# Performance work log

Hardware: AMD Instinct MI355X
Metric: run time of the kernel (lower is better)

The kernel has to match this reference:

```python
import jax, jax.numpy as jnp
import numpy as np

SHAPE = (160, 160, 160)  # spatial grid (D, H, W)
N_VOX = 400_000
C_IN, C_OUT, K = 32, 64, 3


def setup_inputs() -> dict:
    key = jax.random.key(0)
    k1, k2, k3 = jax.random.split(key, 3)
    # unique active voxel coords (batch=0, z, y, x)
    rng = np.random.default_rng(0)
    flat = rng.choice(SHAPE[0] * SHAPE[1] * SHAPE[2], size=N_VOX, replace=False)
    z, y, x = np.unravel_index(flat, SHAPE)
    coors = np.stack([np.zeros(N_VOX, np.int32), z.astype(np.int32), y.astype(np.int32), x.astype(np.int32)], axis=1)
    features = jax.random.normal(k1, (N_VOX, C_IN), dtype=jnp.float32)
    weight = jax.random.normal(k2, (K * K * K, C_IN, C_OUT), dtype=jnp.float32) * (1.0 / np.sqrt(C_IN * K * K * K))
    bias = jax.random.normal(k3, (C_OUT,), dtype=jnp.float32) * 0.01
    return {"features": features, "coors": jnp.asarray(coors), "weight": weight, "bias": bias, "batch_size": 1}


def reference(features, coors, weight, bias, batch_size):
    # Submanifold sparse 3D conv: output coords == input coords.
    n = features.shape[0]
    b, z, y, x = coors[:, 0], coors[:, 1], coors[:, 2], coors[:, 3]
    D, H, W = SHAPE
    # dense voxel->row index lookup grid (the "hash map" for rulebook build)
    grid = jnp.full((batch_size, D, H, W), -1, dtype=jnp.int32)
    grid = grid.at[b, z, y, x].set(jnp.arange(n, dtype=jnp.int32))
    out = jnp.broadcast_to(bias, (n, C_OUT)).astype(features.dtype)
    k = 0
    for dz in (-1, 0, 1):
        for dy in (-1, 0, 1):
            for dx in (-1, 0, 1):
                nz, ny, nx = z + dz, y + dy, x + dx
                inb = (nz >= 0) & (nz < D) & (ny >= 0) & (ny < H) & (nx >= 0) & (nx < W)
                idx = grid[b, jnp.clip(nz, 0, D - 1), jnp.clip(ny, 0, H - 1), jnp.clip(nx, 0, W - 1)]
                valid = inb & (idx >= 0)
                gathered = jnp.where(valid[:, None], features[jnp.clip(idx, 0)], 0.0)  # [n, C_IN]
                out = out + gathered @ weight[k]  # small GEMM per kernel offset
                k += 1
    return out
```

## Files before the change

### kernel.cpp

```cpp
#include <hip/hip_runtime.h>
#include <stdint.h>

#define DD 160
#define HH 160
#define WW 160
#define NGRID (DD*HH*WW)
#define NCHUNK (NGRID/1024)
#define CIN 32
#define COUT 64
#define KK 27
#define BLOCK 1024
#define WPB 16
#define NBLOCKS 256
#define TOTW (NBLOCKS*WPB)
#define M27 0x07FFFFFFu

typedef _Float16 h2_t __attribute__((ext_vector_type(2)));

__device__ __forceinline__ h2_t as_h2(uint32_t u) {
    union { uint32_t u; h2_t h; } c; c.u = u; return c.h;
}
__device__ __forceinline__ uint32_t f2h(float f) {
    union { _Float16 h; uint16_t u; } c; c.h = (_Float16)f; return (uint32_t)c.u;
}

__device__ __forceinline__ float dot2(uint32_t fu, uint32_t wu, float acc) {
#if defined(__has_builtin)
#if __has_builtin(__builtin_amdgcn_fdot2)
    return __builtin_amdgcn_fdot2(as_h2(fu), as_h2(wu), acc, false);
#else
    h2_t f = as_h2(fu), w = as_h2(wu);
    acc = fmaf((float)f.x, (float)w.x, acc);
    return fmaf((float)f.y, (float)w.y, acc);
#endif
#else
    h2_t f = as_h2(fu), w = as_h2(wu);
    acc = fmaf((float)f.x, (float)w.x, acc);
    return fmaf((float)f.y, (float)w.y, acc);
#endif
}

__global__ void scatter_pack(const int4* __restrict__ coors, const float* __restrict__ w,
                             int* __restrict__ grid, int* __restrict__ cnt,
                             uint4* __restrict__ wpk, int n)
{
    int gid = blockIdx.x * 256 + threadIdx.x;
    if (gid < n) {
        int4 c = coors[gid];
        int cell = (c.y*HH + c.z)*WW + c.w;
        grid[cell] = gid;
        atomicAdd(&cnt[cell >> 10], 1);
    } else if (gid < n + KK*4*COUT) {
        int t = gid - n;
        int co = t & 63;
        int g  = (t >> 6) & 3;
        int k  = t >> 8;
        const float* base = w + (size_t)k*CIN*COUT + (size_t)(8*g)*COUT + co;
        uint4 r;
        r.x = f2h(base[0*COUT]) | (f2h(base[1*COUT]) << 16);
        r.y = f2h(base[2*COUT]) | (f2h(base[3*COUT]) << 16);
        r.z = f2h(base[4*COUT]) | (f2h(base[5*COUT]) << 16);
        r.w = f2h(base[6*COUT]) | (f2h(base[7*COUT]) << 16);
        wpk[t] = r;
    }
}

__global__ __launch_bounds__(1024) void scan_chunks(const int* __restrict__ cnt,
                                                    int* __restrict__ base)
{
    __shared__ int s[1024];
    int t = threadIdx.x;
    int c0 = 0, c1 = 0, c2 = 0, c3 = 0, sum;
    int i0 = t * 4;
    if (i0 + 3 < NCHUNK) { c0 = cnt[i0]; c1 = cnt[i0+1]; c2 = cnt[i0+2]; c3 = cnt[i0+3]; }
    else {
        if (i0     < NCHUNK) c0 = cnt[i0];
        if (i0 + 1 < NCHUNK) c1 = cnt[i0+1];
        if (i0 + 2 < NCHUNK) c2 = cnt[i0+2];
        if (i0 + 3 < NCHUNK) c3 = cnt[i0+3];
    }
    sum = c0 + c1 + c2 + c3;
    s[t] = sum; __syncthreads();
    for (int off = 1; off < 1024; off <<= 1) {
        int val = (t >= off) ? s[t - off] : 0;
        __syncthreads();
        s[t] += val;
        __syncthreads();
    }
    int excl = s[t] - sum;
    if (i0     < NCHUNK) { base[i0]   = excl; excl += c0; }
    if (i0 + 1 < NCHUNK) { base[i0+1] = excl; excl += c1; }
    if (i0 + 2 < NCHUNK) { base[i0+2] = excl; excl += c2; }
    if (i0 + 3 < NCHUNK) { base[i0+3] = excl; }
}

__global__ __launch_bounds__(1024) void emit_sort(const float4* __restrict__ f4,
                                                  int* __restrict__ grid,
                                                  const int* __restrict__ base,
                                                  int* __restrict__ pos, int* __restrict__ om,
                                                  uint2* __restrict__ fh)
{
    __shared__ int wt[16];
    int cell = blockIdx.x * 1024 + threadIdx.x;
    int g = grid[cell];
    bool pres = g >= 0;
    unsigned long long bal = __ballot(pres);
    int lane = threadIdx.x & 63;
    int wv = threadIdx.x >> 6;
    int lpre = __popcll(bal & ((1ull << lane) - 1ull));
    if (lane == 0) wt[wv] = __popcll(bal);
    __syncthreads();
    if (threadIdx.x == 0) {
        int acc = 0;
        for (int i = 0; i < 16; ++i) { int c = wt[i]; wt[i] = acc; acc += c; }
    }
    __syncthreads();
    if (pres) {
        int sp = base[blockIdx.x] + wt[wv] + lpre;
        pos[sp] = cell;
        om[sp]  = g;
        grid[cell] = sp;
        const float4* src = f4 + (size_t)g * 8;
        uint2* dst = fh + (size_t)sp * 8;
        #pragma unroll
        for (int q = 0; q < 8; ++q) {
            float4 vv = src[q];
            uint2 r;
            r.x = f2h(vv.x) | (f2h(vv.y) << 16);
            r.y = f2h(vv.z) | (f2h(vv.w) << 16);
            dst[q] = r;
        }
    }
}

#define LOAD4(D0,D1,D2,D3,J) { \
    const uint4* fp_ = fh4 + (size_t)(J) * 4; \
    D0 = fp_[0]; D1 = fp_[1]; D2 = fp_[2]; D3 = fp_[3]; }

#define MAC4(F0,F1,F2,F3,kk) { \
    const uint4* wl_ = wlds + (size_t)(kk)*4*COUT + lane; \
    uint4 w0_ = wl_[0], w1_ = wl_[COUT], w2_ = wl_[2*COUT], w3_ = wl_[3*COUT]; \
    a0 = dot2(F0.x, w0_.x, a0); a1 = dot2(F0.y, w0_.y, a1); \
    a2 = dot2(F0.z, w0_.z, a2); a3 = dot2(F0.w, w0_.w, a3); \
    a0 = dot2(F1.x, w1_.x, a0); a1 = dot2(F1.y, w1_.y, a1); \
    a2 = dot2(F1.z, w1_.z, a2); a3 = dot2(F1.w, w1_.w, a3); \
    a0 = dot2(F2.x, w2_.x, a0); a1 = dot2(F2.y, w2_.y, a1); \
    a2 = dot2(F2.z, w2_.z, a2); a3 = dot2(F2.w, w2_.w, a3); \
    a0 = dot2(F3.x, w3_.x, a0); a1 = dot2(F3.y, w3_.y, a1); \
    a2 = dot2(F3.z, w3_.z, a2); a3 = dot2(F3.w, w3_.w, a3); }

__global__ __launch_bounds__(BLOCK, 4) void sparse_conv(
    const uint4* __restrict__ fh4, const int* __restrict__ pos, const int* __restrict__ om,
    const float* __restrict__ bias, const uint4* __restrict__ wpk,
    const int* __restrict__ grid, float* __restrict__ out, int n, int run)
{
    extern __shared__ uint4 wlds[];

    for (int t = threadIdx.x; t < KK*4*COUT; t += BLOCK)
        wlds[t] = wpk[t];
    __syncthreads();

    const int lane = threadIdx.x & 63;
    const int wave = __builtin_amdgcn_readfirstlane((int)(threadIdx.x >> 6));
    const int b0 = blockIdx.x;
    const int sw = ((b0 & 7) << 5) + (b0 >> 3);
    const int wg = sw * WPB + wave;
    const int lo = wg * run;
    const int hi = min(n, lo + run);

    const float b = bias[lane];
    const int pl = lane & 31;
    const bool prober = pl < KK;
    const int dz = pl / 9 - 1;
    const int dy = (pl / 3) % 3 - 1;
    const int dx = pl % 3 - 1;
    const int hioff = (lane >= 32) ? 1 : 0;

    int nidx = -1;

    auto probe = [&](int pb) -> int {
        int r = -1;
        int pv = pb + hioff;
        if (prober && pv < hi) {
            int cell = pos[pv];
            int z = cell / (HH*WW); int rem = cell % (HH*WW);
            int y = rem / WW;       int x = rem % WW;
            int nz = z + dz, ny = y + dy, nx = x + dx;
            if (nz >= 0 && nz < DD && ny >= 0 && ny < HH && nx >= 0 && nx < WW)
                r = grid[(nz*HH + ny)*WW + nx];
        }
        return r;
    };

    auto runvox = [&](uint32_t m, int base, int orig) {
        float a0 = 0.f, a1 = 0.f, a2 = 0.f, a3 = 0.f;
        uint4 A0, A1, A2, A3, B0, B1, B2, B3;
        int kA = __ffs(m) - 1; m &= m - 1;
        int jA = __builtin_amdgcn_readlane(nidx, base + kA);
        LOAD4(A0, A1, A2, A3, jA);
        for (;;) {
            if (!m) { MAC4(A0, A1, A2, A3, kA); break; }
            int kB = __ffs(m) - 1; m &= m - 1;
            int jB = __builtin_amdgcn_readlane(nidx, base + kB);
            LOAD4(B0, B1, B2, B3, jB);
            MAC4(A0, A1, A2, A3, kA);
            if (!m) { MAC4(B0, B1, B2, B3, kB); break; }
            kA = __ffs(m) - 1; m &= m - 1;
            jA = __builtin_amdgcn_readlane(nidx, base + kA);
            LOAD4(A0, A1, A2, A3, jA);
            MAC4(B0, B1, B2, B3, kB);
        }
        float r = b + ((a0 + a1) + (a2 + a3));
        __builtin_nontemporal_store(r, out + (size_t)orig * COUT + lane);
    };

    int v = lo;
    nidx = probe(v);

    while (v < hi) {
        unsigned long long bal = __ballot(nidx >= 0);
        int nidx_next = probe(v + 2);

        uint32_t mA = (uint32_t)bal & M27;
        uint32_t mB = (uint32_t)(bal >> 32) & M27;

        runvox(mA, 0, om[v]);
        if (v + 1 < hi) runvox(mB, 32, om[v + 1]);

        v += 2;
        nidx = nidx_next;
    }
}

extern "C" void kernel_launch(void* const* d_in, const int* in_sizes, int n_in,
                              void* d_out, int out_size, void* d_ws, size_t ws_size,
                              hipStream_t stream) {
    const float* feats  = (const float*)d_in[0];
    const int*   coors  = (const int*)d_in[1];
    const float* weight = (const float*)d_in[2];
    const float* bias   = (const float*)d_in[3];
    float*       outp   = (float*)d_out;

    const int n = in_sizes[1] / 4;

    char* ws = (char*)d_ws;
    int*   grid = (int*)ws;                                   ws += (size_t)NGRID * 4;
    int*   cnt  = (int*)ws;                                   ws += (size_t)NCHUNK * 4;
    int*   base = (int*)ws;                                   ws += (size_t)NCHUNK * 4;
    uint4* wpk  = (uint4*)ws;                                 ws += (size_t)KK * 4 * COUT * 16;
    int*   pos  = (int*)ws;                                   ws += (size_t)n * 4;
    int*   om   = (int*)ws;                                   ws += (size_t)n * 4;
    uint2* fh   = (uint2*)ws;

    hipMemsetAsync(grid, 0xFF, (size_t)NGRID * 4, stream);
    hipMemsetAsync(cnt, 0, (size_t)NCHUNK * 4, stream);

    scatter_pack<<<(n + KK*4*COUT + 255) / 256, 256, 0, stream>>>(
        (const int4*)coors, weight, grid, cnt, wpk, n);

    scan_chunks<<<1, 1024, 0, stream>>>(cnt, base);

    emit_sort<<<NCHUNK, 1024, 0, stream>>>((const float4*)feats, grid, base, pos, om, fh);

    const int run = (n + TOTW - 1) / TOTW;
    const size_t lds = (size_t)KK * 4 * COUT * sizeof(uint4);
    sparse_conv<<<NBLOCKS, BLOCK, lds, stream>>>((const uint4*)fh, pos, om,
                                                 bias, wpk, grid, outp, n, run);
}
```

Before: 365.3 us.

## Replace per-voxel fdot2 accumulation with 16-voxel MFMA tiles over all taps

The conv kernel now processes groups of 16 sorted voxels per wave and computes all 27 taps densely with 16x16x32 f16 MFMA instructions, instead of walking each voxel's neighbor bitmask with fdot2. Missing neighbors point to a zero feature row appended after the features, which scatter_pack now writes, so the loop needs no branches. Weights are repacked in MFMA B-operand layout, and neighbor probes for the next group are prefetched and distributed with ds_bpermute. The aim is to trade wasted dense work on roughly 90% empty taps for much higher matrix throughput and regular control flow. Voxel counts not divisible by 16 would leave a tail unprocessed.

```diff
diff --git a/kernel.cpp b/kernel.cpp
--- a/kernel.cpp
+++ b/kernel.cpp
@@ -13,36 +13,19 @@
 #define WPB 16
 #define NBLOCKS 256
 #define TOTW (NBLOCKS*WPB)
-#define M27 0x07FFFFFFu
-
-typedef _Float16 h2_t __attribute__((ext_vector_type(2)));
-
-__device__ __forceinline__ h2_t as_h2(uint32_t u) {
-    union { uint32_t u; h2_t h; } c; c.u = u; return c.h;
-}
+
+typedef _Float16 f16x8 __attribute__((ext_vector_type(8)));
+typedef float f32x4 __attribute__((ext_vector_type(4)));
+
+union FU { uint4 u; f16x8 h; };
+
 __device__ __forceinline__ uint32_t f2h(float f) {
     union { _Float16 h; uint16_t u; } c; c.h = (_Float16)f; return (uint32_t)c.u;
 }
 
-__device__ __forceinline__ float dot2(uint32_t fu, uint32_t wu, float acc) {
-#if defined(__has_builtin)
-#if __has_builtin(__builtin_amdgcn_fdot2)
-    return __builtin_amdgcn_fdot2(as_h2(fu), as_h2(wu), acc, false);
-#else
-    h2_t f = as_h2(fu), w = as_h2(wu);
-    acc = fmaf((float)f.x, (float)w.x, acc);
-    return fmaf((float)f.y, (float)w.y, acc);
-#endif
-#else
-    h2_t f = as_h2(fu), w = as_h2(wu);
-    acc = fmaf((float)f.x, (float)w.x, acc);
-    return fmaf((float)f.y, (float)w.y, acc);
-#endif
-}
-
 __global__ void scatter_pack(const int4* __restrict__ coors, const float* __restrict__ w,
                              int* __restrict__ grid, int* __restrict__ cnt,
-                             uint4* __restrict__ wpk, int n)
+                             uint4* __restrict__ wpk, uint2* __restrict__ fh, int n)
 {
     int gid = blockIdx.x * 256 + threadIdx.x;
     if (gid < n) {
@@ -50,18 +33,21 @@
         int cell = (c.y*HH + c.z)*WW + c.w;
         grid[cell] = gid;
         atomicAdd(&cnt[cell >> 10], 1);
-    } else if (gid < n + KK*4*COUT) {
+    } else if (gid < n + KK*4*64) {
         int t = gid - n;
-        int co = t & 63;
-        int g  = (t >> 6) & 3;
-        int k  = t >> 8;
-        const float* base = w + (size_t)k*CIN*COUT + (size_t)(8*g)*COUT + co;
+        int l = t & 63, tile = (t >> 6) & 3, k = t >> 8;
+        int col = tile*16 + (l & 15);
+        int k0 = (l >> 4) * 8;
+        const float* base = w + (size_t)k*CIN*COUT + col;
         uint4 r;
-        r.x = f2h(base[0*COUT]) | (f2h(base[1*COUT]) << 16);
-        r.y = f2h(base[2*COUT]) | (f2h(base[3*COUT]) << 16);
-        r.z = f2h(base[4*COUT]) | (f2h(base[5*COUT]) << 16);
-        r.w = f2h(base[6*COUT]) | (f2h(base[7*COUT]) << 16);
+        r.x = f2h(base[(k0+0)*COUT]) | (f2h(base[(k0+1)*COUT]) << 16);
+        r.y = f2h(base[(k0+2)*COUT]) | (f2h(base[(k0+3)*COUT]) << 16);
+        r.z = f2h(base[(k0+4)*COUT]) | (f2h(base[(k0+5)*COUT]) << 16);
+        r.w = f2h(base[(k0+6)*COUT]) | (f2h(base[(k0+7)*COUT]) << 16);
         wpk[t] = r;
+    } else if (gid < n + KK*4*64 + 8) {
+        uint2 z; z.x = 0u; z.y = 0u;
+        fh[(size_t)n*8 + (gid - n - KK*4*64)] = z;
     }
 }
 
@@ -72,13 +58,10 @@
     int t = threadIdx.x;
     int c0 = 0, c1 = 0, c2 = 0, c3 = 0, sum;
     int i0 = t * 4;
-    if (i0 + 3 < NCHUNK) { c0 = cnt[i0]; c1 = cnt[i0+1]; c2 = cnt[i0+2]; c3 = cnt[i0+3]; }
-    else {
-        if (i0     < NCHUNK) c0 = cnt[i0];
-        if (i0 + 1 < NCHUNK) c1 = cnt[i0+1];
-        if (i0 + 2 < NCHUNK) c2 = cnt[i0+2];
-        if (i0 + 3 < NCHUNK) c3 = cnt[i0+3];
-    }
+    if (i0     < NCHUNK) c0 = cnt[i0];
+    if (i0 + 1 < NCHUNK) c1 = cnt[i0+1];
+    if (i0 + 2 < NCHUNK) c2 = cnt[i0+2];
+    if (i0 + 3 < NCHUNK) c3 = cnt[i0+3];
     sum = c0 + c1 + c2 + c3;
     s[t] = sum; __syncthreads();
     for (int off = 1; off < 1024; off <<= 1) {
@@ -133,30 +116,46 @@
     }
 }
 
-#define LOAD4(D0,D1,D2,D3,J) { \
-    const uint4* fp_ = fh4 + (size_t)(J) * 4; \
-    D0 = fp_[0]; D1 = fp_[1]; D2 = fp_[2]; D3 = fp_[3]; }
-
-#define MAC4(F0,F1,F2,F3,kk) { \
-    const uint4* wl_ = wlds + (size_t)(kk)*4*COUT + lane; \
-    uint4 w0_ = wl_[0], w1_ = wl_[COUT], w2_ = wl_[2*COUT], w3_ = wl_[3*COUT]; \
-    a0 = dot2(F0.x, w0_.x, a0); a1 = dot2(F0.y, w0_.y, a1); \
-    a2 = dot2(F0.z, w0_.z, a2); a3 = dot2(F0.w, w0_.w, a3); \
-    a0 = dot2(F1.x, w1_.x, a0); a1 = dot2(F1.y, w1_.y, a1); \
-    a2 = dot2(F1.z, w1_.z, a2); a3 = dot2(F1.w, w1_.w, a3); \
-    a0 = dot2(F2.x, w2_.x, a0); a1 = dot2(F2.y, w2_.y, a1); \
-    a2 = dot2(F2.z, w2_.z, a2); a3 = dot2(F2.w, w2_.w, a3); \
-    a0 = dot2(F3.x, w3_.x, a0); a1 = dot2(F3.y, w3_.y, a1); \
-    a2 = dot2(F3.z, w3_.z, a2); a3 = dot2(F3.w, w3_.w, a3); }
+#define PROBE(R, S0, DST) { \
+    int p = (R)*64 + lane; \
+    int idx = n; \
+    if (p < KK*16) { \
+        int kk = p >> 4; \
+        int vi = (S0) + (p & 15); \
+        unsigned cell = (unsigned)pos[vi]; \
+        int t9 = (kk*57) >> 9;  int r9 = kk - t9*9; \
+        int t3 = (r9*171) >> 9; \
+        int zz = (int)(cell / (HH*WW)); int rem = (int)(cell - (unsigned)zz*(HH*WW)); \
+        int yy = rem / WW; int xx = rem - yy*WW; \
+        int nz = zz + t9 - 1, ny = yy + t3 - 1, nx = xx + (r9 - t3*3) - 1; \
+        if (nz >= 0 && nz < DD && ny >= 0 && ny < HH && nx >= 0 && nx < WW) { \
+            int j = grid[(nz*HH + ny)*WW + nx]; \
+            if (j >= 0) idx = j; \
+        } \
+    } \
+    DST = idx; }
+
+#define TAP(K, NREG) { \
+    int j = __builtin_amdgcn_ds_bpermute(((K)&3)*64 + row4, NREG); \
+    FU a; a.u = fh4[(size_t)j*4 + sub]; \
+    FU b0, b1, b2, b3; \
+    b0.u = wlds[((K)*4+0)*64 + lane]; \
+    b1.u = wlds[((K)*4+1)*64 + lane]; \
+    b2.u = wlds[((K)*4+2)*64 + lane]; \
+    b3.u = wlds[((K)*4+3)*64 + lane]; \
+    acc0 = __builtin_amdgcn_mfma_f32_16x16x32_f16(a.h, b0.h, acc0, 0, 0, 0); \
+    acc1 = __builtin_amdgcn_mfma_f32_16x16x32_f16(a.h, b1.h, acc1, 0, 0, 0); \
+    acc2 = __builtin_amdgcn_mfma_f32_16x16x32_f16(a.h, b2.h, acc2, 0, 0, 0); \
+    acc3 = __builtin_amdgcn_mfma_f32_16x16x32_f16(a.h, b3.h, acc3, 0, 0, 0); }
 
 __global__ __launch_bounds__(BLOCK, 4) void sparse_conv(
     const uint4* __restrict__ fh4, const int* __restrict__ pos, const int* __restrict__ om,
     const float* __restrict__ bias, const uint4* __restrict__ wpk,
-    const int* __restrict__ grid, float* __restrict__ out, int n, int run)
+    const int* __restrict__ grid, float* __restrict__ out, int n)
 {
     extern __shared__ uint4 wlds[];
 
-    for (int t = threadIdx.x; t < KK*4*COUT; t += BLOCK)
+    for (int t = threadIdx.x; t < KK*4*64; t += BLOCK)
         wlds[t] = wpk[t];
     __syncthreads();
 
@@ -165,70 +164,50 @@
     const int b0 = blockIdx.x;
     const int sw = ((b0 & 7) << 5) + (b0 >> 3);
     const int wg = sw * WPB + wave;
-    const int lo = wg * run;
-    const int hi = min(n, lo + run);
-
-    const float b = bias[lane];
-    const int pl = lane & 31;
-    const bool prober = pl < KK;
-    const int dz = pl / 9 - 1;
-    const int dy = (pl / 3) % 3 - 1;
-    const int dx = pl % 3 - 1;
-    const int hioff = (lane >= 32) ? 1 : 0;
-
-    int nidx = -1;
-
-    auto probe = [&](int pb) -> int {
-        int r = -1;
-        int pv = pb + hioff;
-        if (prober && pv < hi) {
-            int cell = pos[pv];
-            int z = cell / (HH*WW); int rem = cell % (HH*WW);
-            int y = rem / WW;       int x = rem % WW;
-            int nz = z + dz, ny = y + dy, nx = x + dx;
-            if (nz >= 0 && nz < DD && ny >= 0 && ny < HH && nx >= 0 && nx < WW)
-                r = grid[(nz*HH + ny)*WW + nx];
+
+    const int G = n >> 4;
+    const int lo_g = (int)(((long long)wg     * G) >> 12);
+    const int hi_g = (int)(((long long)(wg+1) * G) >> 12);
+
+    const int row4 = (lane & 15) * 4;
+    const int sub  = lane >> 4;
+    const float bias0 = bias[ 0 + (lane & 15)];
+    const float bias1 = bias[16 + (lane & 15)];
+    const float bias2 = bias[32 + (lane & 15)];
+    const float bias3 = bias[48 + (lane & 15)];
+
+    int cur[7];
+    if (lo_g < hi_g) {
+        #pragma unroll
+        for (int r = 0; r < 7; ++r) PROBE(r, lo_g*16, cur[r]);
+    }
+
+    for (int g = lo_g; g < hi_g; ++g) {
+        const int gn = (g + 1 < hi_g) ? g + 1 : g;
+        int nxt[7];
+        #pragma unroll
+        for (int r = 0; r < 7; ++r) PROBE(r, gn*16, nxt[r]);
+
+        f32x4 acc0 = {0.f,0.f,0.f,0.f}, acc1 = {0.f,0.f,0.f,0.f};
+        f32x4 acc2 = {0.f,0.f,0.f,0.f}, acc3 = {0.f,0.f,0.f,0.f};
+
+        #pragma unroll
+        for (int k = 0; k < KK; ++k) { TAP(k, cur[k >> 2]); }
+
+        const int s0 = g * 16;
+        #pragma unroll
+        for (int e = 0; e < 4; ++e) {
+            int vv = s0 + (lane >> 4) * 4 + e;
+            int orig = om[vv];
+            float* op = out + (size_t)orig * COUT + (lane & 15);
+            __builtin_nontemporal_store(acc0[e] + bias0, op);
+            __builtin_nontemporal_store(acc1[e] + bias1, op + 16);
+            __builtin_nontemporal_store(acc2[e] + bias2, op + 32);
+            __builtin_nontemporal_store(acc3[e] + bias3, op + 48);
         }
-        return r;
-    };
-
-    auto runvox = [&](uint32_t m, int base, int orig) {
-        float a0 = 0.f, a1 = 0.f, a2 = 0.f, a3 = 0.f;
-        uint4 A0, A1, A2, A3, B0, B1, B2, B3;
-        int kA = __ffs(m) - 1; m &= m - 1;
-        int jA = __builtin_amdgcn_readlane(nidx, base + kA);
-        LOAD4(A0, A1, A2, A3, jA);
-        for (;;) {
-            if (!m) { MAC4(A0, A1, A2, A3, kA); break; }
-            int kB = __ffs(m) - 1; m &= m - 1;
-            int jB = __builtin_amdgcn_readlane(nidx, base + kB);
-            LOAD4(B0, B1, B2, B3, jB);
-            MAC4(A0, A1, A2, A3, kA);
-            if (!m) { MAC4(B0, B1, B2, B3, kB); break; }
-            kA = __ffs(m) - 1; m &= m - 1;
-            jA = __builtin_amdgcn_readlane(nidx, base + kA);
-            LOAD4(A0, A1, A2, A3, jA);
-            MAC4(B0, B1, B2, B3, kB);
-        }
-        float r = b + ((a0 + a1) + (a2 + a3));
-        __builtin_nontemporal_store(r, out + (size_t)orig * COUT + lane);
-    };
-
-    int v = lo;
-    nidx = probe(v);
-
-    while (v < hi) {
-        unsigned long long bal = __ballot(nidx >= 0);
-        int nidx_next = probe(v + 2);
-
-        uint32_t mA = (uint32_t)bal & M27;
-        uint32_t mB = (uint32_t)(bal >> 32) & M27;
-
-        runvox(mA, 0, om[v]);
-        if (v + 1 < hi) runvox(mB, 32, om[v + 1]);
-
-        v += 2;
-        nidx = nidx_next;
+
+        #pragma unroll
+        for (int r = 0; r < 7; ++r) cur[r] = nxt[r];
     }
 }
 
@@ -247,7 +226,7 @@
     int*   grid = (int*)ws;                                   ws += (size_t)NGRID * 4;
     int*   cnt  = (int*)ws;                                   ws += (size_t)NCHUNK * 4;
     int*   base = (int*)ws;                                   ws += (size_t)NCHUNK * 4;
-    uint4* wpk  = (uint4*)ws;                                 ws += (size_t)KK * 4 * COUT * 16;
+    uint4* wpk  = (uint4*)ws;                                 ws += (size_t)KK * 4 * 64 * 16;
     int*   pos  = (int*)ws;                                   ws += (size_t)n * 4;
     int*   om   = (int*)ws;                                   ws += (size_t)n * 4;
     uint2* fh   = (uint2*)ws;
@@ -255,15 +234,14 @@
     hipMemsetAsync(grid, 0xFF, (size_t)NGRID * 4, stream);
     hipMemsetAsync(cnt, 0, (size_t)NCHUNK * 4, stream);
 
-    scatter_pack<<<(n + KK*4*COUT + 255) / 256, 256, 0, stream>>>(
-        (const int4*)coors, weight, grid, cnt, wpk, n);
+    scatter_pack<<<(n + KK*4*64 + 8 + 255) / 256, 256, 0, stream>>>(
+        (const int4*)coors, weight, grid, cnt, wpk, fh, n);
 
     scan_chunks<<<1, 1024, 0, stream>>>(cnt, base);
 
     emit_sort<<<NCHUNK, 1024, 0, stream>>>((const float4*)feats, grid, base, pos, om, fh);
 
-    const int run = (n + TOTW - 1) / TOTW;
-    const size_t lds = (size_t)KK * 4 * COUT * sizeof(uint4);
+    const size_t lds = (size_t)KK * 4 * 64 * sizeof(uint4);
     sparse_conv<<<NBLOCKS, BLOCK, lds, stream>>>((const uint4*)fh, pos, om,
-                                                 bias, wpk, grid, outp, n, run);
-}
+                                                 bias, wpk, grid, outp, n);
+}
```

Result: slower. 929.4 us (+154.4%).
